# Kernel optimization log

Measured on AMD Instinct MI355X. Metric: run time of the kernel, lower is better.

The kernel has to match this reference:

```python
import jax, jax.numpy as jnp
import numpy as np

MARGIN = 1.0
EPS = 1e-6  # torch F.pairwise_distance default eps
B, C, D = 16384, 1000, 1024


def setup_inputs() -> dict:
    key = jax.random.key(0)
    k1, k2, k3 = jax.random.split(key, 3)
    inputs = jax.random.normal(k1, (B, D), dtype=jnp.float32)
    labels = jax.random.randint(k2, (B,), 0, C, dtype=jnp.int64)
    target = jax.random.normal(k3, (C, D), dtype=jnp.float32)
    return {"inputs": inputs, "labels": labels, "target": target}


def _pairdist(a, b):
    # torch F.pairwise_distance(p=2): ||a - b + eps||_2 along last dim
    d = a - b + EPS
    return jnp.sqrt(jnp.sum(d * d, axis=-1))


def reference(inputs, labels, target):
    # --- negative mining: full [B, C] distance matrix via GEMM identity ---
    # (eps is a uniform per-component shift; it does not change the argmin in practice,
    #  and mining indices are non-differentiable anyway)
    x2 = jnp.sum(inputs * inputs, axis=-1, keepdims=True)          # [B, 1]
    t2 = jnp.sum(target * target, axis=-1)                          # [C]
    d2 = x2 - 2.0 * (inputs @ target.T) + t2[None, :]               # [B, C]
    d2 = jnp.maximum(d2, 0.0)
    # exclude the anchor's own class (tx == anchor_label skipped in torch loop)
    own = jax.nn.one_hot(labels, C, dtype=jnp.bool_)                 # [B, C]
    d2 = jnp.where(own, jnp.inf, d2)
    neg_idx = jnp.argmin(d2, axis=-1)                                # [B]

    positive = target[labels]                                        # [B, D]
    negative = target[neg_idx]                                       # [B, D]

    d_ap = _pairdist(inputs, positive)                               # [B]
    d_an = _pairdist(inputs, negative)                               # [B]
    per_anchor = jnp.maximum(d_ap - d_an + MARGIN, 0.0)
    # every anchor forms a valid triplet (C > 1), so total/valid == mean
    return jnp.mean(per_anchor)
```

## Files before the change

### kernel.cpp

```cpp
#include <hip/hip_runtime.h>
#include <hip/hip_bf16.h>

#define NB 16384
#define NC 1000
#define NCP 1024
#define ND 1024
#define BM 128
#define BN 256
#define KSTEPS 32
#define NCB 4

typedef __attribute__((ext_vector_type(8))) short bf16x8;
typedef __attribute__((ext_vector_type(4))) float f32x4;

typedef __attribute__((address_space(1))) const void GV;
typedef __attribute__((address_space(3))) void LV;

__device__ __forceinline__ unsigned short f2bf(float f) {
  union { float f; unsigned u; } c; c.f = f;
  unsigned b = c.u;
  return (unsigned short)((b + 0x7fffu + ((b >> 16) & 1u)) >> 16);
}
__device__ __forceinline__ unsigned pk2(float lo, float hi) {
  return ((unsigned)f2bf(hi) << 16) | (unsigned)f2bf(lo);
}

__global__ __launch_bounds__(256) void prep_kernel(const float* __restrict__ Tf,
                                                   unsigned short* __restrict__ Tb,
                                                   float* __restrict__ t2) {
  const int c = blockIdx.x;
  const int tid = threadIdx.x;
  if (c >= NC) {
    ushort4 z; z.x = z.y = z.z = z.w = 0;
    ((ushort4*)(Tb + (size_t)c * ND))[tid] = z;
    if (tid == 0) t2[c] = 1e30f;
    return;
  }
  float4 v = ((const float4*)(Tf + (size_t)c * ND))[tid];
  float ss = v.x * v.x + v.y * v.y + v.z * v.z + v.w * v.w;
  ushort4 o;
  o.x = f2bf(v.x); o.y = f2bf(v.y); o.z = f2bf(v.z); o.w = f2bf(v.w);
  ((ushort4*)(Tb + (size_t)c * ND))[tid] = o;
  #pragma unroll
  for (int m = 1; m < 64; m <<= 1) ss += __shfl_xor(ss, m, 64);
  __shared__ float red[4];
  if ((tid & 63) == 0) red[tid >> 6] = ss;
  __syncthreads();
  if (tid == 0) t2[c] = red[0] + red[1] + red[2] + red[3];
}

__global__ __launch_bounds__(512, 4) void mine2_kernel(
    const float* __restrict__ X, const int* __restrict__ labels,
    const unsigned short* __restrict__ Tb, const float* __restrict__ t2g,
    float* __restrict__ x2g, float* __restrict__ slab, float2* __restrict__ pairs) {
  __shared__ char sA[2][BM * 64];
  __shared__ char sB[2][BN * 64];
  __shared__ int sLab[BM];
  __shared__ float2 sMin[BM][4];

  const int tid = threadIdx.x;
  const int lane = tid & 63;
  const int wid = tid >> 6;
  const int l15 = lane & 15, l4 = lane >> 4;
  const int wr = wid >> 2, wc = wid & 3;
  const int rb = (int)blockIdx.x >> 2, cb = (int)blockIdx.x & 3;
  const int rowbase = rb * BM, colbase = cb * BN;

  if (tid < BM) sLab[tid] = labels[rowbase + tid];

  const int arow = tid >> 2;
  const float* aptr = X + (size_t)(rowbase + arow) * ND + ((tid & 3) << 3);
  float ss = 0.0f;

  f32x4 acc[4][4] = {};
  int cur = 0;

  auto stage = [&](int buf, int ks) {
    #pragma unroll
    for (int i = 0; i < 2; ++i) {
      const int o = i * 8192 + tid * 16;
      const char* src = (const char*)Tb + (size_t)(colbase + (o >> 6)) * 2048 + ks * 64 + (o & 63);
      __builtin_amdgcn_global_load_lds((GV*)src, (LV*)(sB[buf] + o), 16, 0, 0);
    }
    float4 v0 = *(const float4*)(aptr + ks * 32);
    float4 v1 = *(const float4*)(aptr + ks * 32 + 4);
    if (cb == 0) {
      ss += v0.x * v0.x + v0.y * v0.y + v0.z * v0.z + v0.w * v0.w
          + v1.x * v1.x + v1.y * v1.y + v1.z * v1.z + v1.w * v1.w;
    }
    uint4 w;
    w.x = pk2(v0.x, v0.y); w.y = pk2(v0.z, v0.w);
    w.z = pk2(v1.x, v1.y); w.w = pk2(v1.z, v1.w);
    *(uint4*)(sA[buf] + tid * 16) = w;
  };

  stage(0, 0);
  for (int ks = 0; ks < KSTEPS; ++ks) {
    __syncthreads();
    if (ks + 1 < KSTEPS) stage(cur ^ 1, ks + 1);
    const char* pa = sA[cur];
    const char* pb = sB[cur];
    bf16x8 af[4];
    #pragma unroll
    for (int m = 0; m < 4; ++m)
      af[m] = *(const bf16x8*)(pa + ((wr * 64 + m * 16 + l15) * 64 + l4 * 16));
    #pragma unroll
    for (int n = 0; n < 4; ++n) {
      bf16x8 bfr = *(const bf16x8*)(pb + ((wc * 64 + n * 16 + l15) * 64 + l4 * 16));
      #pragma unroll
      for (int m = 0; m < 4; ++m)
        acc[m][n] = __builtin_amdgcn_mfma_f32_16x16x32_bf16(af[m], bfr, acc[m][n], 0, 0, 0);
    }
    cur ^= 1;
  }

  if (cb == 0) {
    ss += __shfl_xor(ss, 1, 64);
    ss += __shfl_xor(ss, 2, 64);
    if ((tid & 3) == 0) x2g[rowbase + arow] = ss;
  }

  float t2v[4];
  #pragma unroll
  for (int n = 0; n < 4; ++n) t2v[n] = t2g[colbase + wc * 64 + n * 16 + l15];

  #pragma unroll
  for (int m = 0; m < 4; ++m) {
    #pragma unroll
    for (int j = 0; j < 4; ++j) {
      const int rowl = wr * 64 + m * 16 + l4 * 4 + j;
      const int lab = sLab[rowl];
      float bv = 3.0e38f; int bi = 0x7fffffff;
      #pragma unroll
      for (int n = 0; n < 4; ++n) {
        const int col = colbase + wc * 64 + n * 16 + l15;
        const float sc = t2v[n] - 2.0f * acc[m][n][j];
        if (col == lab) slab[rowbase + rowl] = sc;
        const float sce = (col == lab) ? 3.2e38f : sc;
        if (sce < bv || (sce == bv && col < bi)) { bv = sce; bi = col; }
      }
      #pragma unroll
      for (int mk = 1; mk < 16; mk <<= 1) {
        const float ov = __shfl_xor(bv, mk, 64);
        const int   oi = __shfl_xor(bi, mk, 64);
        if (ov < bv || (ov == bv && oi < bi)) { bv = ov; bi = oi; }
      }
      if (l15 == 0) sMin[rowl][wc] = make_float2(bv, __int_as_float(bi));
    }
  }
  __syncthreads();
  if (tid < BM) {
    float2 p = sMin[tid][0];
    #pragma unroll
    for (int q = 1; q < 4; ++q) {
      float2 o = sMin[tid][q];
      if (o.x < p.x || (o.x == p.x && __float_as_int(o.y) < __float_as_int(p.y))) p = o;
    }
    pairs[(size_t)(rowbase + tid) * NCB + cb] = p;
  }
}

__global__ __launch_bounds__(256) void finalize_kernel(
    const float2* __restrict__ pairs, const float* __restrict__ slab,
    const float* __restrict__ x2g, float* __restrict__ out) {
  const int r = blockIdx.x * 256 + threadIdx.x;
  float2 p = pairs[(size_t)r * NCB];
  #pragma unroll
  for (int q = 1; q < NCB; ++q) {
    float2 o = pairs[(size_t)r * NCB + q];
    if (o.x < p.x || (o.x == p.x && __float_as_int(o.y) < __float_as_int(p.y))) p = o;
  }
  const float x2v = x2g[r];
  const float dap = sqrtf(fmaxf(x2v + slab[r], 0.0f));
  const float dan = sqrtf(fmaxf(x2v + p.x, 0.0f));
  float h = fmaxf(dap - dan + 1.0f, 0.0f);
  #pragma unroll
  for (int mk = 1; mk < 64; mk <<= 1) h += __shfl_xor(h, mk, 64);
  __shared__ float red[4];
  if ((threadIdx.x & 63) == 0) red[threadIdx.x >> 6] = h;
  __syncthreads();
  if (threadIdx.x == 0)
    atomicAdd(out, (red[0] + red[1] + red[2] + red[3]) * (1.0f / (float)NB));
}

extern "C" void kernel_launch(void* const* d_in, const int* in_sizes, int n_in,
                              void* d_out, int out_size, void* d_ws, size_t ws_size,
                              hipStream_t stream) {
  const float* X = (const float*)d_in[0];
  const int* labels = (const int*)d_in[1];
  const float* Tf = (const float*)d_in[2];
  float* out = (float*)d_out;

  char* ws = (char*)d_ws;
  unsigned short* Tb = (unsigned short*)ws;
  float* t2   = (float*)(ws + 2097152);
  float* x2   = (float*)(ws + 2097152 + 4096);
  float* slab = (float*)(ws + 2097152 + 4096 + 65536);
  float2* pairs = (float2*)(ws + 2097152 + 4096 + 131072);

  hipMemsetAsync(d_out, 0, sizeof(float), stream);
  prep_kernel<<<NCP, 256, 0, stream>>>(Tf, Tb, t2);
  mine2_kernel<<<(NB / BM) * NCB, 512, 0, stream>>>(X, labels, Tb, t2, x2, slab, pairs);
  finalize_kernel<<<NB / 256, 256, 0, stream>>>(pairs, slab, x2, out);
}
```

Baseline: 153.9 us.

## Halve row tile, prefetch A into registers, custom waitcnt barrier, remap workgroups

Shrinks the mining GEMM tile to 64 rows with 256-thread blocks and four column waves. A is prefetched two k-steps ahead in registers, and the __syncthreads is replaced by a hand-placed s_waitcnt vmcnt(2)/s_barrier so global loads stay in flight across the barrier. Workgroup IDs are remapped so that consecutive blocks spread across row groups, which is meant to improve cache locality and XCD distribution. The cost is more blocks, each reloading the B tile, and the raw waitcnt carries a synchronisation-correctness risk.

```diff
diff --git a/kernel.cpp b/kernel.cpp
--- a/kernel.cpp
+++ b/kernel.cpp
@@ -5,7 +5,7 @@
 #define NC 1000
 #define NCP 1024
 #define ND 1024
-#define BM 128
+#define BM 64
 #define BN 256
 #define KSTEPS 32
 #define NCB 4
@@ -49,7 +49,7 @@
   if (tid == 0) t2[c] = red[0] + red[1] + red[2] + red[3];
 }
 
-__global__ __launch_bounds__(512, 4) void mine2_kernel(
+__global__ __launch_bounds__(256, 3) void mine3_kernel(
     const float* __restrict__ X, const int* __restrict__ labels,
     const unsigned short* __restrict__ Tb, const float* __restrict__ t2g,
     float* __restrict__ x2g, float* __restrict__ slab, float2* __restrict__ pairs) {
@@ -60,50 +60,67 @@
 
   const int tid = threadIdx.x;
   const int lane = tid & 63;
-  const int wid = tid >> 6;
+  const int wc = tid >> 6;
   const int l15 = lane & 15, l4 = lane >> 4;
-  const int wr = wid >> 2, wc = wid & 3;
-  const int rb = (int)blockIdx.x >> 2, cb = (int)blockIdx.x & 3;
+
+  const int bid = (int)blockIdx.x;
+  const int wgid = (bid & 7) * 128 + (bid >> 3);
+  const int rb = wgid >> 2, cb = wgid & 3;
   const int rowbase = rb * BM, colbase = cb * BN;
 
   if (tid < BM) sLab[tid] = labels[rowbase + tid];
 
-  const int arow = tid >> 2;
-  const float* aptr = X + (size_t)(rowbase + arow) * ND + ((tid & 3) << 3);
+  const float* aptr = X + (size_t)(rowbase + (tid >> 2)) * ND + ((tid & 3) << 3);
   float ss = 0.0f;
-
-  f32x4 acc[4][4] = {};
-  int cur = 0;
-
-  auto stage = [&](int buf, int ks) {
-    #pragma unroll
-    for (int i = 0; i < 2; ++i) {
-      const int o = i * 8192 + tid * 16;
-      const char* src = (const char*)Tb + (size_t)(colbase + (o >> 6)) * 2048 + ks * 64 + (o & 63);
-      __builtin_amdgcn_global_load_lds((GV*)src, (LV*)(sB[buf] + o), 16, 0, 0);
-    }
-    float4 v0 = *(const float4*)(aptr + ks * 32);
-    float4 v1 = *(const float4*)(aptr + ks * 32 + 4);
+  float4 rA0, rA1;
+
+  auto loadA = [&](int kt) {
+    rA0 = *(const float4*)(aptr + kt * 32);
+    rA1 = *(const float4*)(aptr + kt * 32 + 4);
+  };
+  auto writeA = [&](int buf) {
     if (cb == 0) {
-      ss += v0.x * v0.x + v0.y * v0.y + v0.z * v0.z + v0.w * v0.w
-          + v1.x * v1.x + v1.y * v1.y + v1.z * v1.z + v1.w * v1.w;
+      ss += rA0.x * rA0.x + rA0.y * rA0.y + rA0.z * rA0.z + rA0.w * rA0.w
+          + rA1.x * rA1.x + rA1.y * rA1.y + rA1.z * rA1.z + rA1.w * rA1.w;
     }
     uint4 w;
-    w.x = pk2(v0.x, v0.y); w.y = pk2(v0.z, v0.w);
-    w.z = pk2(v1.x, v1.y); w.w = pk2(v1.z, v1.w);
+    w.x = pk2(rA0.x, rA0.y); w.y = pk2(rA0.z, rA0.w);
+    w.z = pk2(rA1.x, rA1.y); w.w = pk2(rA1.z, rA1.w);
     *(uint4*)(sA[buf] + tid * 16) = w;
   };
-
-  stage(0, 0);
+  auto stageB = [&](int buf, int kt) {
+    #pragma unroll
+    for (int i = 0; i < 4; ++i) {
+      const int o = i * 4096 + tid * 16;
+      const char* src = (const char*)Tb + (size_t)(colbase + (o >> 6)) * 2048 + kt * 64 + (o & 63);
+      __builtin_amdgcn_global_load_lds((GV*)src, (LV*)(sB[buf] + o), 16, 0, 0);
+    }
+  };
+
+  f32x4 acc[4][4] = {};
+
+  loadA(0);
+  stageB(0, 0);
+  writeA(0);
+  loadA(1);
+  __builtin_amdgcn_sched_barrier(0);
+  asm volatile("s_waitcnt vmcnt(2) lgkmcnt(0)\n\ts_barrier" ::: "memory");
+  __builtin_amdgcn_sched_barrier(0);
+
+  int cur = 0;
   for (int ks = 0; ks < KSTEPS; ++ks) {
-    __syncthreads();
-    if (ks + 1 < KSTEPS) stage(cur ^ 1, ks + 1);
+    if (ks + 1 < KSTEPS) {
+      writeA(cur ^ 1);
+      stageB(cur ^ 1, ks + 1);
+      const int kn = (ks + 2 < KSTEPS) ? ks + 2 : KSTEPS - 1;
+      loadA(kn);
+    }
     const char* pa = sA[cur];
     const char* pb = sB[cur];
     bf16x8 af[4];
     #pragma unroll
     for (int m = 0; m < 4; ++m)
-      af[m] = *(const bf16x8*)(pa + ((wr * 64 + m * 16 + l15) * 64 + l4 * 16));
+      af[m] = *(const bf16x8*)(pa + ((m * 16 + l15) * 64 + l4 * 16));
     #pragma unroll
     for (int n = 0; n < 4; ++n) {
       bf16x8 bfr = *(const bf16x8*)(pb + ((wc * 64 + n * 16 + l15) * 64 + l4 * 16));
@@ -111,13 +128,16 @@
       for (int m = 0; m < 4; ++m)
         acc[m][n] = __builtin_amdgcn_mfma_f32_16x16x32_bf16(af[m], bfr, acc[m][n], 0, 0, 0);
     }
+    __builtin_amdgcn_sched_barrier(0);
+    asm volatile("s_waitcnt vmcnt(2) lgkmcnt(0)\n\ts_barrier" ::: "memory");
+    __builtin_amdgcn_sched_barrier(0);
     cur ^= 1;
   }
 
   if (cb == 0) {
     ss += __shfl_xor(ss, 1, 64);
     ss += __shfl_xor(ss, 2, 64);
-    if ((tid & 3) == 0) x2g[rowbase + arow] = ss;
+    if ((tid & 3) == 0) x2g[rowbase + (tid >> 2)] = ss;
   }
 
   float t2v[4];
@@ -128,7 +148,7 @@
   for (int m = 0; m < 4; ++m) {
     #pragma unroll
     for (int j = 0; j < 4; ++j) {
-      const int rowl = wr * 64 + m * 16 + l4 * 4 + j;
+      const int rowl = m * 16 + l4 * 4 + j;
       const int lab = sLab[rowl];
       float bv = 3.0e38f; int bi = 0x7fffffff;
       #pragma unroll
@@ -200,6 +220,6 @@
 
   hipMemsetAsync(d_out, 0, sizeof(float), stream);
   prep_kernel<<<NCP, 256, 0, stream>>>(Tf, Tb, t2);
-  mine2_kernel<<<(NB / BM) * NCB, 512, 0, stream>>>(X, labels, Tb, t2, x2, slab, pairs);
+  mine3_kernel<<<(NB / BM) * NCB, 256, 0, stream>>>(X, labels, Tb, t2, x2, slab, pairs);
   finalize_kernel<<<NB / 256, 256, 0, stream>>>(pairs, slab, x2, out);
 }
```

Result: slower. 180.9 us (+17.5%).

## Pre-convert inputs to bf16 in a separate pass and stage both operands via direct-to-LDS loads

Applied to the files above, without the earlier changes.

Adds a prepx kernel that converts X to bf16 and computes row norms once, then a new mining GEMM that loads both A and B tiles with global_load_lds instead of each of the four column blocks re-reading fp32 X and converting in registers. It also remaps block IDs so blocks sharing a row tile are spread across XCDs. This trades an extra 32MB bf16 write plus a read for halving GEMM-side X traffic and removing conversion work from the main loop. It depends on a workspace large enough for the bf16 copy and falls back otherwise.

```diff
diff --git a/kernel.cpp b/kernel.cpp
--- a/kernel.cpp
+++ b/kernel.cpp
@@ -49,6 +49,122 @@
   if (tid == 0) t2[c] = red[0] + red[1] + red[2] + red[3];
 }
 
+__global__ __launch_bounds__(256) void prepx_kernel(const float* __restrict__ X,
+                                                    unsigned short* __restrict__ Xb,
+                                                    float* __restrict__ x2) {
+  const int r = blockIdx.x;
+  const int tid = threadIdx.x;
+  float4 v = ((const float4*)(X + (size_t)r * ND))[tid];
+  float ss = v.x * v.x + v.y * v.y + v.z * v.z + v.w * v.w;
+  ushort4 o;
+  o.x = f2bf(v.x); o.y = f2bf(v.y); o.z = f2bf(v.z); o.w = f2bf(v.w);
+  ((ushort4*)(Xb + (size_t)r * ND))[tid] = o;
+  #pragma unroll
+  for (int m = 1; m < 64; m <<= 1) ss += __shfl_xor(ss, m, 64);
+  __shared__ float red[4];
+  if ((tid & 63) == 0) red[tid >> 6] = ss;
+  __syncthreads();
+  if (tid == 0) x2[r] = red[0] + red[1] + red[2] + red[3];
+}
+
+__global__ __launch_bounds__(512, 4) void mine4_kernel(
+    const unsigned short* __restrict__ Xb, const int* __restrict__ labels,
+    const unsigned short* __restrict__ Tb, const float* __restrict__ t2g,
+    float* __restrict__ slab, float2* __restrict__ pairs) {
+  __shared__ char sA[2][BM * 64];
+  __shared__ char sB[2][BN * 64];
+  __shared__ int sLab[BM];
+  __shared__ float2 sMin[BM][4];
+
+  const int tid = threadIdx.x;
+  const int lane = tid & 63;
+  const int wid = tid >> 6;
+  const int l15 = lane & 15, l4 = lane >> 4;
+  const int wr = wid >> 2, wc = wid & 3;
+
+  const int bid = (int)blockIdx.x;
+  const int wgid = (bid & 7) * 64 + (bid >> 3);
+  const int rb = wgid >> 2, cb = wgid & 3;
+  const int rowbase = rb * BM, colbase = cb * BN;
+
+  if (tid < BM) sLab[tid] = labels[rowbase + tid];
+
+  auto stage = [&](int buf, int ks) {
+    {
+      const int o = tid * 16;
+      const char* src = (const char*)Xb + (size_t)(rowbase + (o >> 6)) * 2048 + ks * 64 + (o & 63);
+      __builtin_amdgcn_global_load_lds((GV*)src, (LV*)(sA[buf] + o), 16, 0, 0);
+    }
+    #pragma unroll
+    for (int i = 0; i < 2; ++i) {
+      const int o = i * 8192 + tid * 16;
+      const char* src = (const char*)Tb + (size_t)(colbase + (o >> 6)) * 2048 + ks * 64 + (o & 63);
+      __builtin_amdgcn_global_load_lds((GV*)src, (LV*)(sB[buf] + o), 16, 0, 0);
+    }
+  };
+
+  f32x4 acc[4][4] = {};
+  stage(0, 0);
+  int cur = 0;
+  for (int ks = 0; ks < KSTEPS; ++ks) {
+    __syncthreads();
+    if (ks + 1 < KSTEPS) stage(cur ^ 1, ks + 1);
+    const char* pa = sA[cur];
+    const char* pb = sB[cur];
+    bf16x8 af[4];
+    #pragma unroll
+    for (int m = 0; m < 4; ++m)
+      af[m] = *(const bf16x8*)(pa + ((wr * 64 + m * 16 + l15) * 64 + l4 * 16));
+    #pragma unroll
+    for (int n = 0; n < 4; ++n) {
+      bf16x8 bfr = *(const bf16x8*)(pb + ((wc * 64 + n * 16 + l15) * 64 + l4 * 16));
+      #pragma unroll
+      for (int m = 0; m < 4; ++m)
+        acc[m][n] = __builtin_amdgcn_mfma_f32_16x16x32_bf16(af[m], bfr, acc[m][n], 0, 0, 0);
+    }
+    cur ^= 1;
+  }
+
+  float t2v[4];
+  #pragma unroll
+  for (int n = 0; n < 4; ++n) t2v[n] = t2g[colbase + wc * 64 + n * 16 + l15];
+
+  #pragma unroll
+  for (int m = 0; m < 4; ++m) {
+    #pragma unroll
+    for (int j = 0; j < 4; ++j) {
+      const int rowl = wr * 64 + m * 16 + l4 * 4 + j;
+      const int lab = sLab[rowl];
+      float bv = 3.0e38f; int bi = 0x7fffffff;
+      #pragma unroll
+      for (int n = 0; n < 4; ++n) {
+        const int col = colbase + wc * 64 + n * 16 + l15;
+        const float sc = t2v[n] - 2.0f * acc[m][n][j];
+        if (col == lab) slab[rowbase + rowl] = sc;
+        const float sce = (col == lab) ? 3.2e38f : sc;
+        if (sce < bv || (sce == bv && col < bi)) { bv = sce; bi = col; }
+      }
+      #pragma unroll
+      for (int mk = 1; mk < 16; mk <<= 1) {
+        const float ov = __shfl_xor(bv, mk, 64);
+        const int   oi = __shfl_xor(bi, mk, 64);
+        if (ov < bv || (ov == bv && oi < bi)) { bv = ov; bi = oi; }
+      }
+      if (l15 == 0) sMin[rowl][wc] = make_float2(bv, __int_as_float(bi));
+    }
+  }
+  __syncthreads();
+  if (tid < BM) {
+    float2 p = sMin[tid][0];
+    #pragma unroll
+    for (int q = 1; q < 4; ++q) {
+      float2 o = sMin[tid][q];
+      if (o.x < p.x || (o.x == p.x && __float_as_int(o.y) < __float_as_int(p.y))) p = o;
+    }
+    pairs[(size_t)(rowbase + tid) * NCB + cb] = p;
+  }
+}
+
 __global__ __launch_bounds__(512, 4) void mine2_kernel(
     const float* __restrict__ X, const int* __restrict__ labels,
     const unsigned short* __restrict__ Tb, const float* __restrict__ t2g,
@@ -197,9 +313,17 @@
   float* x2   = (float*)(ws + 2097152 + 4096);
   float* slab = (float*)(ws + 2097152 + 4096 + 65536);
   float2* pairs = (float2*)(ws + 2097152 + 4096 + 131072);
+  unsigned short* Xb = (unsigned short*)(ws + 2756608);
+
+  const size_t NEED = 2756608u + (size_t)NB * ND * 2u;
 
   hipMemsetAsync(d_out, 0, sizeof(float), stream);
   prep_kernel<<<NCP, 256, 0, stream>>>(Tf, Tb, t2);
-  mine2_kernel<<<(NB / BM) * NCB, 512, 0, stream>>>(X, labels, Tb, t2, x2, slab, pairs);
+  if (ws_size >= NEED) {
+    prepx_kernel<<<NB, 256, 0, stream>>>(X, Xb, x2);
+    mine4_kernel<<<(NB / BM) * NCB, 512, 0, stream>>>(Xb, labels, Tb, t2, slab, pairs);
+  } else {
+    mine2_kernel<<<(NB / BM) * NCB, 512, 0, stream>>>(X, labels, Tb, t2, x2, slab, pairs);
+  }
   finalize_kernel<<<NB / 256, 256, 0, stream>>>(pairs, slab, x2, out);
 }
```

After: 150.2 us. 1.02x faster.
